# Kernel tuning notes

Measured on AMD Instinct MI355X. Metric: run time of the kernel, lower is better.

Reference implementation:

```python
import jax, jax.numpy as jnp
import numpy as np

N_NODES = 20000
N_EDGES = 240000
N_GRAPHS = 200
D_IN = 118
H = 256          # simplified hidden width standing in for the mul=50 irreps hidden
NB = 10          # number_of_basis
RH = 100         # fc_neurons hidden
L = 3            # layers
SH = 9           # lmax=2 -> 1+3+5 spherical-harmonic channels
MAX_RADIUS = 5.0
NUM_NEIGHBORS = 12.0


def setup_inputs() -> dict:
    key = jax.random.key(0)
    ks = jax.random.split(key, 16)
    inp = {
        "x": jax.random.normal(ks[0], (N_NODES, D_IN), jnp.float32),
        "pos": jax.random.normal(ks[1], (N_NODES, 3), jnp.float32),
        "edge_shift": jax.random.normal(ks[2], (N_EDGES, 3), jnp.float32),
        "lattice": jax.random.normal(ks[3], (N_GRAPHS, 3, 3), jnp.float32),
        "W_embed": jax.random.normal(ks[4], (D_IN, H), jnp.float32) / np.sqrt(D_IN),
        "r1": jax.random.normal(ks[5], (L, NB, RH), jnp.float32) / np.sqrt(NB),
        "b1": jax.random.normal(ks[6], (L, RH), jnp.float32) * 0.1,
        "r2": jax.random.normal(ks[7], (L, RH, H), jnp.float32) / np.sqrt(RH),
        "Wtp": jax.random.normal(ks[8], (L, SH, H, H), jnp.float32) / np.sqrt(SH * H),
        "Wself": jax.random.normal(ks[9], (L, H, H), jnp.float32) / np.sqrt(H),
        "Wskip": jax.random.normal(ks[10], (L, H, H), jnp.float32) / np.sqrt(H),
        "Wout": jax.random.normal(ks[11], (H, 1), jnp.float32) / np.sqrt(H),
        "edge_index": jax.random.randint(ks[12], (2, N_EDGES), 0, N_NODES, jnp.int64)
                        if jax.config.jax_enable_x64 else
                      jax.random.randint(ks[12], (2, N_EDGES), 0, N_NODES).astype(jnp.int32),
        "batch": jnp.sort(jax.random.randint(ks[13], (N_NODES,), 0, N_GRAPHS)).astype(jnp.int32),
    }
    return inp


def _sph_harm_lmax2(u):
    """Component-normalized real spherical harmonics up to l=2 on unit vectors u [E,3]."""
    x, y, z = u[:, 0], u[:, 1], u[:, 2]
    c1 = np.sqrt(3.0)
    c2 = np.sqrt(15.0)
    return jnp.stack([
        jnp.ones_like(x),                       # l=0
        c1 * x, c1 * y, c1 * z,                 # l=1
        c2 * x * y, c2 * y * z,                 # l=2
        (np.sqrt(5.0) / 2.0) * (3.0 * z * z - 1.0),
        c2 * x * z, (c2 / 2.0) * (x * x - y * y),
    ], axis=1)                                  # [E, 9]


def _soft_one_hot_cosine(lens):
    """e3nn soft_one_hot_linspace(basis='cosine', cutoff=True) * sqrt(NB)."""
    vals = jnp.linspace(0.0, MAX_RADIUS, NB + 2)
    step = vals[1] - vals[0]
    vals = vals[1:-1]
    diff = (lens[:, None] - vals[None, :]) / step          # [E, NB]
    emb = jnp.cos(0.5 * jnp.pi * diff) * (diff > -1.0) * (diff < 1.0)
    return emb * np.sqrt(float(NB))


def _forward(x, pos, edge_shift, lattice, W_embed, r1, b1, r2, Wtp, Wself, Wskip, Wout,
             edge_src, edge_dst, batch):
    edge_batch = batch[edge_src]                            # [E]
    # periodic edge vectors: pos[dst] - pos[src] + shift @ lattice[graph]
    edge_vec = pos[edge_dst] - pos[edge_src] + jnp.einsum(
        'ni,nij->nj', edge_shift, lattice[edge_batch])      # [E, 3]
    lens = jnp.linalg.norm(edge_vec, axis=1)                # [E]
    u = edge_vec / (lens[:, None] + 1e-12)
    sh = _sph_harm_lmax2(u)                                 # [E, 9]
    emb = _soft_one_hot_cosine(lens)                        # [E, NB]

    h = x @ W_embed                                         # [N, H]
    inv_sqrt_deg = 1.0 / np.sqrt(NUM_NEIGHBORS)
    for l in range(L):
        radial = jax.nn.silu(emb @ r1[l] + b1[l]) @ r2[l]   # [E, H]
        hs = h[edge_src] * radial                           # gather + radial gate
        # weighted tensor-product-like message: sum_a (hs * sh_a) @ Wtp[l, a]
        msg = (hs * sh[:, 0:1]) @ Wtp[l, 0]
        for a in range(1, SH):
            msg = msg + (hs * sh[:, a:a + 1]) @ Wtp[l, a]   # [E, H]
        agg = jax.ops.segment_sum(msg, edge_dst, num_segments=N_NODES) * inv_sqrt_deg
        h = jax.nn.gelu(agg @ Wself[l] + h @ Wskip[l])      # [N, H]

    node_out = h @ Wout                                     # [N, 1]
    # scatter_mean over graphs
    sums = jax.ops.segment_sum(node_out, batch, num_segments=N_GRAPHS)
    cnts = jax.ops.segment_sum(jnp.ones((N_NODES, 1), node_out.dtype), batch,
                               num_segments=N_GRAPHS)
    return sums / jnp.maximum(cnts, 1.0)                    # [G, 1]


def reference(x, pos, edge_shift, lattice, W_embed, r1, b1, r2, Wtp, Wself, Wskip, Wout,
              edge_index, batch):
    return _forward(x, pos, edge_shift, lattice, W_embed, r1, b1, r2, Wtp, Wself, Wskip,
                    Wout, edge_index[0], edge_index[1], batch)
```

## Files before the change

kernel.cpp:

```cpp
#include <hip/hip_runtime.h>
#include <hip/hip_bf16.h>
#include <cstddef>
#include <cstdint>

#define NNODE  20000
#define MPAD   20096
#define NEDGE  240000
#define NGRAPH 200
#define DIN    118
#define HD     256
#define NBASIS 10
#define RHID   100
#define NLAYER 3
#define NSH    9
#define SHSTR  16
#define KTP    (NSH * HD)
#define KTOT   (KTP + HD)
#define KR2    128
#define KEMB   128
#define NRT    (MPAD / 64)

typedef _Float16 f16;
typedef _Float16 f16x2 __attribute__((ext_vector_type(2)));
typedef _Float16 f16x4 __attribute__((ext_vector_type(4)));
typedef _Float16 f16x8 __attribute__((ext_vector_type(8)));
typedef float    f32x4 __attribute__((ext_vector_type(4)));

__device__ __forceinline__ float gelu_tanh(float v) {
  float v3 = v * v * v;
  return 0.5f * v * (1.f + tanhf(0.7978845608028654f * (v + 0.044715f * v3)));
}

__device__ __forceinline__ void gload16(const void* g, void* l) {
  __builtin_amdgcn_global_load_lds(
      (const __attribute__((address_space(1))) unsigned int*)g,
      (__attribute__((address_space(3))) unsigned int*)l, 16, 0, 0);
}

__device__ __forceinline__ int perm64(int rho) {
  return (rho & ~63) | ((rho & 15) * 4 + ((rho >> 4) & 3));
}
__device__ __forceinline__ int inv_perm64(int n) {
  return (n & ~63) | (((n & 3) << 4) | ((n >> 2) & 15));
}

__global__ void deg_hist_kernel(const int* __restrict__ ei, int* __restrict__ deg)
{
  int e = blockIdx.x * 256 + threadIdx.x;
  if (e >= NEDGE) return;
  atomicAdd(&deg[ei[NEDGE + e]], 1);
}

__global__ void scan_kernel(const int* __restrict__ deg, int* __restrict__ rowptr)
{
  __shared__ int part[256];
  int t = threadIdx.x;
  const int chunk = (NNODE + 255) / 256;
  int start = t * chunk;
  int end = min(start + chunk, NNODE);
  int s = 0;
  for (int i = start; i < end; ++i) s += deg[i];
  part[t] = s;
  __syncthreads();
  for (int off = 1; off < 256; off <<= 1) {
    int v = (t >= off) ? part[t - off] : 0;
    __syncthreads();
    part[t] += v;
    __syncthreads();
  }
  int run = (t == 0) ? 0 : part[t - 1];
  for (int i = start; i < end; ++i) { rowptr[i] = run; run += deg[i]; }
  if (t == 255) rowptr[NNODE] = run;
}

__global__ void edge_geom_kernel(const float* __restrict__ pos,
                                 const float* __restrict__ shift,
                                 const float* __restrict__ lat,
                                 const int* __restrict__ ei,
                                 const int* __restrict__ batch,
                                 const int* __restrict__ rowptr,
                                 int* __restrict__ cursor,
                                 f16* __restrict__ sh_s,
                                 float* __restrict__ lens_s)
{
  int e = blockIdx.x * 256 + threadIdx.x;
  if (e >= NEDGE) return;
  int src = ei[e];
  int dst = ei[NEDGE + e];
  int b = batch[src];
  const float* L = lat + (size_t)b * 9;
  float s0 = shift[e * 3 + 0], s1 = shift[e * 3 + 1], s2 = shift[e * 3 + 2];
  float ev[3];
#pragma unroll
  for (int j = 0; j < 3; ++j)
    ev[j] = pos[dst * 3 + j] - pos[src * 3 + j] + s0 * L[j] + s1 * L[3 + j] + s2 * L[6 + j];
  float len = sqrtf(ev[0] * ev[0] + ev[1] * ev[1] + ev[2] * ev[2]);
  float inv = 1.f / (len + 1e-12f);
  float x = ev[0] * inv, y = ev[1] * inv, z = ev[2] * inv;
  const float c1 = 1.7320508075688772f;
  const float c2 = 3.872983346207417f;
  int p = atomicAdd(&cursor[dst], 1);
  int si = rowptr[dst] + p;
  f16* she = sh_s + (size_t)si * SHSTR;
  she[0] = (f16)1.f;
  she[1] = (f16)(c1 * x);
  she[2] = (f16)(c1 * y);
  she[3] = (f16)(c1 * z);
  she[4] = (f16)(c2 * x * y);
  she[5] = (f16)(c2 * y * z);
  she[6] = (f16)(1.1180339887498949f * (3.f * z * z - 1.f));
  she[7] = (f16)(c2 * x * z);
  she[8] = (f16)(1.9364916731037085f * (x * x - y * y));
  she[9] = (f16)0.f;
  *(int*)(she + 10) = src;
  she[12] = (f16)0.f; she[13] = (f16)0.f; she[14] = (f16)0.f; she[15] = (f16)0.f;
  lens_s[si] = len;
}

__global__ void prep_kernel(const float* __restrict__ Wtp_l,
                            const float* __restrict__ Wself_l,
                            const float* __restrict__ Wskip_l,
                            const float* __restrict__ r2l,
                            const float* __restrict__ r1l,
                            const float* __restrict__ b1l,
                            f16* __restrict__ Wtp16,
                            f16* __restrict__ WselfT16,
                            f16* __restrict__ Bcat,
                            f16* __restrict__ r2h,
                            f16* __restrict__ r1h)
{
  int b = blockIdx.x, t = threadIdx.x;
  if (b < KTP) {
    int i = b * 256 + t;
    Wtp16[i] = (f16)Wtp_l[i];
  } else if (b < KTP + 256) {
    int n = b - KTP;
    WselfT16[(size_t)n * HD + t] = (f16)(Wself_l[(size_t)t * HD + n] * 0.28867513459481287f);
  } else if (b < KTP + 512) {
    int rho = b - KTP - 256;
    int pcol = perm64(rho);
    Bcat[(size_t)rho * KTOT + KTP + t] = (f16)Wskip_l[(size_t)t * HD + pcol];
  } else if (b < KTP + 768) {
    int rho = b - KTP - 512;
    if (t < KR2) {
      int p = perm64(rho);
      r2h[(size_t)rho * KR2 + t] = (t < RHID) ? (f16)r2l[(size_t)t * HD + p] : (f16)0.f;
    }
  } else {
#pragma unroll
    for (int u = 0; u < 16; ++u) {
      int idx = u * 256 + t;
      int n = idx >> 5, j = idx & 31;
      float v = 0.f;
      if (n < RHID) {
        if (j < NBASIS) v = r1l[(size_t)j * RHID + n];
        else if (j == NBASIS) v = b1l[n];
      }
      r1h[idx] = (f16)v;
    }
  }
}

__global__ void convert_x_kernel(const float* __restrict__ x, f16* __restrict__ xh)
{
  int i = blockIdx.x * 2 + (threadIdx.x >> 7);
  int k = threadIdx.x & 127;
  xh[(size_t)i * KEMB + k] = (i < NNODE && k < DIN) ? (f16)x[(size_t)i * DIN + k] : (f16)0.f;
}

__global__ void convert_wemb_kernel(const float* __restrict__ Wemb, f16* __restrict__ WembT16)
{
  int n = blockIdx.x, k = threadIdx.x;
  WembT16[(size_t)n * KEMB + k] = (k < DIN) ? (f16)Wemb[(size_t)k * HD + n] : (f16)0.f;
}

__global__ __launch_bounds__(256) void gemm_nt_kernel(
    const f16* __restrict__ A, const f16* __restrict__ B,
    f16* __restrict__ C, int K, int ldc, int permRows)
{
  __shared__ __align__(16) f16 As[4][64][8];
  __shared__ __align__(16) f16 Bs[4][128][8];
  int t = threadIdx.x;
  int lane = t & 63, w = t >> 6;
  int row0 = blockIdx.x * 64;
  int n0 = blockIdx.y * 128;
  f32x4 acc[2][4];
#pragma unroll
  for (int i = 0; i < 2; ++i)
#pragma unroll
    for (int j = 0; j < 4; ++j) acc[i][j] = (f32x4){0.f, 0.f, 0.f, 0.f};
  int mq = (w & 1) * 32, nq = (w >> 1) * 64;
  for (int k0 = 0; k0 < K; k0 += 32) {
    {
      int row = t & 63, cc = t >> 6;
      *(uint4*)&As[cc][row][0] = *(const uint4*)(A + (size_t)(row0 + row) * K + k0 + cc * 8);
    }
#pragma unroll
    for (int u = 0; u < 2; ++u) {
      int idx = t + u * 256;
      int ch = idx >> 7, nn = idx & 127;
      *(uint4*)&Bs[ch][nn][0] = *(const uint4*)(B + (size_t)(n0 + nn) * K + k0 + ch * 8);
    }
    __syncthreads();
    int q = lane >> 4, r = lane & 15;
    f16x8 af[2], bfr[4];
#pragma unroll
    for (int i = 0; i < 2; ++i) af[i] = *(const f16x8*)&As[q][mq + i * 16 + r][0];
#pragma unroll
    for (int j = 0; j < 4; ++j) bfr[j] = *(const f16x8*)&Bs[q][nq + j * 16 + r][0];
#pragma unroll
    for (int i = 0; i < 2; ++i)
#pragma unroll
      for (int j = 0; j < 4; ++j)
        acc[i][j] = __builtin_amdgcn_mfma_f32_16x16x32_f16(af[i], bfr[j], acc[i][j], 0, 0, 0);
    __syncthreads();
  }
  int q4 = ((lane >> 4)) * 4, cl = lane & 15;
#pragma unroll
  for (int i = 0; i < 2; ++i)
#pragma unroll
    for (int rr = 0; rr < 4; ++rr) {
      int row = row0 + mq + i * 16 + q4 + rr;
      int orow = permRows ? inv_perm64(row) : row;
#pragma unroll
      for (int j = 0; j < 4; ++j)
        C[(size_t)orow * ldc + n0 + nq + j * 16 + cl] = (f16)acc[i][j][rr];
    }
}

#define RHSTR 136
__global__ __launch_bounds__(256) void radial_kernel(
    const float* __restrict__ lens_s,
    const f16* __restrict__ r1h,
    const f16* __restrict__ r2h,
    f16* __restrict__ rad)
{
  __shared__ __align__(16) f16 emb_s[64][40];
  __shared__ __align__(16) f16 rhA[64 * RHSTR];
  int t = threadIdx.x;
  int lane = t & 63, w = t >> 6;
  int r = lane & 15, q = lane >> 4;
  int e0 = blockIdx.x * 64;

  {
    float len = lens_s[e0 + lane];
    const float step = 5.f / 11.f;
    const float sq = 3.1622776601683795f;
    f16x8 v;
#pragma unroll
    for (int kk = 0; kk < 8; ++kk) {
      int j = w * 8 + kk;
      float val = 0.f;
      if (j < NBASIS) {
        float d = (len - (float)(j + 1) * step) / step;
        val = (d > -1.f && d < 1.f) ? (__cosf(1.5707963267948966f * d) * sq) : 0.f;
      } else if (j == NBASIS) {
        val = 1.f;
      }
      v[kk] = (f16)val;
    }
    *(f16x8*)&emb_s[lane][w * 8] = v;
  }

  int n0w = w * 64;
  f16x8 bfr[4][4];
#pragma unroll
  for (int j = 0; j < 4; ++j)
#pragma unroll
    for (int ks = 0; ks < 4; ++ks)
      bfr[j][ks] = *(const f16x8*)(r2h + (size_t)(n0w + j * 16 + r) * KR2 + ks * 32 + q * 8);

  f16x8 b1f[2];
#pragma unroll
  for (int j = 0; j < 2; ++j)
    b1f[j] = *(const f16x8*)(r1h + (size_t)((2 * w + j) * 16 + r) * 32 + q * 8);

  __syncthreads();

  f32x4 acc1[4][2];
#pragma unroll
  for (int i = 0; i < 4; ++i)
#pragma unroll
    for (int j = 0; j < 2; ++j) acc1[i][j] = (f32x4){0.f, 0.f, 0.f, 0.f};
  {
    f16x8 a1f[4];
#pragma unroll
    for (int i = 0; i < 4; ++i)
      a1f[i] = *(const f16x8*)&emb_s[i * 16 + r][q * 8];
#pragma unroll
    for (int i = 0; i < 4; ++i)
#pragma unroll
      for (int j = 0; j < 2; ++j)
        acc1[i][j] = __builtin_amdgcn_mfma_f32_16x16x32_f16(a1f[i], b1f[j], acc1[i][j], 0, 0, 0);
  }

#pragma unroll
  for (int i = 0; i < 4; ++i)
#pragma unroll
    for (int j = 0; j < 2; ++j)
#pragma unroll
      for (int rr = 0; rr < 4; ++rr) {
        float s = acc1[i][j][rr];
        s = __fdividef(s, 1.f + __expf(-s));
        rhA[(i * 16 + q * 4 + rr) * RHSTR + (2 * w + j) * 16 + r] = (f16)s;
      }
  __syncthreads();

  f32x4 acc[4][4];
#pragma unroll
  for (int i = 0; i < 4; ++i)
#pragma unroll
    for (int j = 0; j < 4; ++j) acc[i][j] = (f32x4){0.f, 0.f, 0.f, 0.f};
#pragma unroll
  for (int ks = 0; ks < 4; ++ks) {
    f16x8 af[4];
#pragma unroll
    for (int i = 0; i < 4; ++i)
      af[i] = *(const f16x8*)&rhA[(i * 16 + r) * RHSTR + ks * 32 + q * 8];
#pragma unroll
    for (int i = 0; i < 4; ++i)
#pragma unroll
      for (int j = 0; j < 4; ++j)
        acc[i][j] = __builtin_amdgcn_mfma_f32_16x16x32_f16(af[i], bfr[j][ks], acc[i][j], 0, 0, 0);
  }

#pragma unroll
  for (int i = 0; i < 4; ++i)
#pragma unroll
    for (int rr = 0; rr < 4; ++rr) {
      int m = i * 16 + q * 4 + rr;
      f16x4 o;
#pragma unroll
      for (int j = 0; j < 4; ++j) o[j] = (f16)acc[i][j][rr];
      *(f16x4*)(rad + (size_t)(e0 + m) * HD + n0w + r * 4) = o;
    }
}

__global__ __launch_bounds__(256) void gather2_kernel(
    const int* __restrict__ rowptr, const f16* __restrict__ rad,
    const f16* __restrict__ h, const f16* __restrict__ sh_s,
    f16* __restrict__ T)
{
  int t = threadIdx.x;
  int half = t >> 7, lc = t & 127;
  int base = blockIdx.x * 4;
  for (int s = 0; s < 2; ++s) {
    int n = base + s * 2 + half;
    int beg = rowptr[n], end = rowptr[n + 1];
    float a0[NSH], a1[NSH];
#pragma unroll
    for (int a = 0; a < NSH; ++a) { a0[a] = 0.f; a1[a] = 0.f; }
    int j = beg;
    for (; j + 2 <= end; j += 2) {
      const f16* she0 = sh_s + (size_t)j * SHSTR;
      const f16* she1 = she0 + SHSTR;
      f16x8 s80 = *(const f16x8*)she0;
      f16x8 s81 = *(const f16x8*)she1;
      float s8v0 = (float)she0[8];
      float s8v1 = (float)she1[8];
      int src0 = *(const int*)(she0 + 10);
      int src1 = *(const int*)(she1 + 10);
      f16x2 rv0 = *(const f16x2*)(rad + (size_t)j * HD + 2 * lc);
      f16x2 rv1 = *(const f16x2*)(rad + (size_t)(j + 1) * HD + 2 * lc);
      f16x2 hv0 = *(const f16x2*)(h + (size_t)src0 * HD + 2 * lc);
      f16x2 hv1 = *(const f16x2*)(h + (size_t)src1 * HD + 2 * lc);
      float p00 = (float)rv0[0] * (float)hv0[0];
      float p01 = (float)rv0[1] * (float)hv0[1];
      float p10 = (float)rv1[0] * (float)hv1[0];
      float p11 = (float)rv1[1] * (float)hv1[1];
#pragma unroll
      for (int a = 0; a < 8; ++a) {
        float sv0 = (float)s80[a], sv1 = (float)s81[a];
        a0[a] += sv0 * p00 + sv1 * p10;
        a1[a] += sv0 * p01 + sv1 * p11;
      }
      a0[8] += s8v0 * p00 + s8v1 * p10;
      a1[8] += s8v0 * p01 + s8v1 * p11;
    }
    if (j < end) {
      const f16* she = sh_s + (size_t)j * SHSTR;
      f16x8 s8 = *(const f16x8*)she;
      float s8v = (float)she[8];
      int src = *(const int*)(she + 10);
      f16x2 rv = *(const f16x2*)(rad + (size_t)j * HD + 2 * lc);
      f16x2 hv = *(const f16x2*)(h + (size_t)src * HD + 2 * lc);
      float p0 = (float)rv[0] * (float)hv[0];
      float p1 = (float)rv[1] * (float)hv[1];
#pragma unroll
      for (int a = 0; a < 8; ++a) {
        float sv = (float)s8[a];
        a0[a] += sv * p0; a1[a] += sv * p1;
      }
      a0[8] += s8v * p0; a1[8] += s8v * p1;
    }
    f16* Tn = T + (size_t)n * KTP + 2 * lc;
#pragma unroll
    for (int a = 0; a < NSH; ++a) {
      f16x2 o; o[0] = (f16)a0[a]; o[1] = (f16)a1[a];
      *(f16x2*)(Tn + a * HD) = o;
    }
  }
}

#define GBM 64
#define GBN 128
#define NKSTEP (KTOT / 32)
#define NBUF 4
__global__ __launch_bounds__(256) void gemm_fused_kernel(
    const f16* __restrict__ A1,
    const f16* __restrict__ A2,
    const f16* __restrict__ B,
    f16* __restrict__ C)
{
  __shared__ __align__(16) f16 As[NBUF][GBM][4][8];
  __shared__ __align__(16) f16 Bs[NBUF][GBN][4][8];
  int t = threadIdx.x;
  int lane = t & 63, w = t >> 6;
  int row0 = blockIdx.x * GBM;
  int n0 = blockIdx.y * GBN;
  int mq = (w & 1) * 32, nq = (w >> 1) * 64;
  int q = lane >> 4, r = lane & 15;

  int arow = t >> 2;
  int ach = (t & 3) ^ ((t >> 3) & 3);

  f32x4 acc[2][4];
#pragma unroll
  for (int i = 0; i < 2; ++i)
#pragma unroll
    for (int j = 0; j < 4; ++j) acc[i][j] = (f32x4){0.f, 0.f, 0.f, 0.f};

  auto stage = [&](int buf, int k0) {
    const f16* ga = (k0 < KTP)
        ? (A1 + (size_t)(row0 + arow) * KTP + k0 + ach * 8)
        : (A2 + (size_t)(row0 + arow) * HD + (k0 - KTP) + ach * 8);
    gload16(ga, (f16*)As + (size_t)buf * (GBM * 32) + w * 512);
#pragma unroll
    for (int u = 0; u < 2; ++u) {
      int idx = t + u * 256;
      int brow = idx >> 2;
      int bch = (idx & 3) ^ ((idx >> 3) & 3);
      const f16* gb = B + (size_t)(n0 + brow) * KTOT + k0 + bch * 8;
      gload16(gb, (f16*)Bs + (size_t)buf * (GBN * 32) + (u * 256 + w * 64) * 8);
    }
  };

  stage(0, 0);
  stage(1, 32);
  stage(2, 64);

  int swz = (q ^ ((r >> 1) & 3)) * 8;
  int cur = 0;
  for (int s = 0; s < NKSTEP; ++s) {
    if (s <= NKSTEP - 3)      asm volatile("s_waitcnt vmcnt(6)" ::: "memory");
    else if (s == NKSTEP - 2) asm volatile("s_waitcnt vmcnt(3)" ::: "memory");
    else                      asm volatile("s_waitcnt vmcnt(0)" ::: "memory");
    __builtin_amdgcn_s_barrier();
    if (s + 3 < NKSTEP) stage((cur + 3) & 3, (s + 3) * 32);

    const f16* As_c = (const f16*)As + (size_t)cur * (GBM * 32);
    const f16* Bs_c = (const f16*)Bs + (size_t)cur * (GBN * 32);
    f16x8 af[2], bfr[4];
#pragma unroll
    for (int i = 0; i < 2; ++i)
      af[i] = *(const f16x8*)(As_c + (mq + i * 16 + r) * 32 + swz);
#pragma unroll
    for (int j = 0; j < 4; ++j)
      bfr[j] = *(const f16x8*)(Bs_c + (nq + j * 16 + r) * 32 + swz);
#pragma unroll
    for (int i = 0; i < 2; ++i)
#pragma unroll
      for (int j = 0; j < 4; ++j)
        acc[i][j] = __builtin_amdgcn_mfma_f32_16x16x32_f16(af[i], bfr[j], acc[i][j], 0, 0, 0);
    cur = (cur + 1) & 3;
  }

  int q4 = (lane >> 4) * 4, cl = lane & 15;
#pragma unroll
  for (int i = 0; i < 2; ++i)
#pragma unroll
    for (int rr = 0; rr < 4; ++rr) {
      int row = row0 + mq + i * 16 + q4 + rr;
      f16x4 o;
#pragma unroll
      for (int j = 0; j < 4; ++j) o[j] = (f16)gelu_tanh(acc[i][j][rr]);
      *(f16x4*)(C + (size_t)row * HD + n0 + nq + cl * 4) = o;
    }
}

__global__ __launch_bounds__(256) void node_out_fused_kernel(
    const f16* __restrict__ h,
    const float* __restrict__ Wout,
    const int* __restrict__ batch,
    float* __restrict__ out)
{
  __shared__ float red[256];
  int g = blockIdx.x;
  int t = threadIdx.x;
  int lo = 0, hi = NNODE;
  while (lo < hi) { int mid = (lo + hi) >> 1; if (batch[mid] < g) lo = mid + 1; else hi = mid; }
  int start = lo;
  hi = NNODE;
  while (lo < hi) { int mid = (lo + hi) >> 1; if (batch[mid] < g + 1) lo = mid + 1; else hi = mid; }
  int end = lo;
  int half = t >> 7, lc = t & 127;
  float a0 = 0.f, a1 = 0.f;
  for (int n = start + half; n < end; n += 2) {
    f16x2 v = *(const f16x2*)(h + (size_t)n * HD + 2 * lc);
    a0 += (float)v[0];
    a1 += (float)v[1];
  }
  red[t] = a0 * Wout[2 * lc] + a1 * Wout[2 * lc + 1];
  for (int off = 128; off > 0; off >>= 1) {
    __syncthreads();
    if (t < off) red[t] += red[t + off];
  }
  if (t == 0) out[g] = red[0] / fmaxf((float)(end - start), 1.f);
}

extern "C" void kernel_launch(void* const* d_in, const int* in_sizes, int n_in,
                              void* d_out, int out_size, void* d_ws, size_t ws_size,
                              hipStream_t stream)
{
  (void)in_sizes; (void)n_in; (void)out_size;
  const float* x     = (const float*)d_in[0];
  const float* pos   = (const float*)d_in[1];
  const float* shift = (const float*)d_in[2];
  const float* lat   = (const float*)d_in[3];
  const float* Wemb  = (const float*)d_in[4];
  const float* r1    = (const float*)d_in[5];
  const float* b1    = (const float*)d_in[6];
  const float* r2    = (const float*)d_in[7];
  const float* Wtp   = (const float*)d_in[8];
  const float* Wself = (const float*)d_in[9];
  const float* Wskip = (const float*)d_in[10];
  const float* Wout  = (const float*)d_in[11];
  const int*   eidx  = (const int*)d_in[12];
  const int*   batch = (const int*)d_in[13];
  float* out = (float*)d_out;

  char* ws = (char*)d_ws;
  size_t off = 0;
  auto alloc = [&](size_t bytes) -> char* {
    char* p = ws + off;
    off += (bytes + 255) & ~(size_t)255;
    return p;
  };
  f16*   sh_s    = (f16*)alloc((size_t)NEDGE * SHSTR * 2);
  float* lens_s  = (float*)alloc((size_t)NEDGE * 4);
  f16*   hA      = (f16*)alloc((size_t)MPAD * HD * 2);
  f16*   hB      = (f16*)alloc((size_t)MPAD * HD * 2);
  f16*   T       = (f16*)alloc((size_t)MPAD * KTP * 2);
  f16*   rad     = (f16*)alloc((size_t)NEDGE * HD * 2);
  f16*   Bcat    = (f16*)alloc((size_t)HD * KTOT * 2);
  f16*   r2h     = (f16*)alloc((size_t)HD * KR2 * 2);
  f16*   r1hb    = (f16*)alloc((size_t)128 * 32 * 2);
  f16*   Wtp16   = (f16*)alloc((size_t)KTP * HD * 2);
  f16*   WselfT16= (f16*)alloc((size_t)HD * HD * 2);
  int*   rowptr  = (int*)alloc((size_t)(NNODE + 1) * 4);
  int*   deg     = (int*)alloc((size_t)NNODE * 4);
  int*   cursor  = (int*)alloc((size_t)NNODE * 4);
  if (off > ws_size) return;

  f16*   xh      = rad;
  f16*   WembT16 = rad + (size_t)MPAD * KEMB;

  hipMemsetAsync(deg, 0, (size_t)NNODE * 4, stream);
  hipMemsetAsync(cursor, 0, (size_t)NNODE * 4, stream);

  const int EB = (NEDGE + 255) / 256;
  deg_hist_kernel<<<EB, 256, 0, stream>>>(eidx, deg);
  scan_kernel<<<1, 256, 0, stream>>>(deg, rowptr);
  edge_geom_kernel<<<EB, 256, 0, stream>>>(pos, shift, lat, eidx, batch,
                                           rowptr, cursor, sh_s, lens_s);

  convert_x_kernel<<<MPAD / 2, 256, 0, stream>>>(x, xh);
  convert_wemb_kernel<<<HD, KEMB, 0, stream>>>(Wemb, WembT16);
  {
    dim3 eg(MPAD / 64, HD / 128);
    gemm_nt_kernel<<<eg, 256, 0, stream>>>(xh, WembT16, hA, KEMB, HD, 0);
  }

  f16* hcur = hA;
  f16* hnxt = hB;
  dim3 fgrid(NRT, 2);
  dim3 wgrid(HD / 64, KTP / 128);
  for (int l = 0; l < NLAYER; ++l) {
    const float* r1l = r1 + (size_t)l * NBASIS * RHID;
    const float* b1l = b1 + (size_t)l * RHID;
    const float* r2l = r2 + (size_t)l * RHID * HD;
    const float* Wtp_l = Wtp + (size_t)l * NSH * HD * HD;
    const float* Wself_l = Wself + (size_t)l * HD * HD;
    const float* Wskip_l = Wskip + (size_t)l * HD * HD;

    prep_kernel<<<KTP + 768 + 1, 256, 0, stream>>>(Wtp_l, Wself_l, Wskip_l, r2l,
                                                   r1l, b1l,
                                                   Wtp16, WselfT16, Bcat, r2h, r1hb);
    gemm_nt_kernel<<<wgrid, 256, 0, stream>>>(WselfT16, Wtp16, Bcat, HD, KTOT, 1);

    radial_kernel<<<NEDGE / 64, 256, 0, stream>>>(lens_s, r1hb, r2h, rad);
    gather2_kernel<<<NNODE / 4, 256, 0, stream>>>(rowptr, rad, hcur, sh_s, T);
    gemm_fused_kernel<<<fgrid, 256, 0, stream>>>(T, hcur, Bcat, hnxt);
    f16* tmp = hcur; hcur = hnxt; hnxt = tmp;
  }

  node_out_fused_kernel<<<NGRAPH, 256, 0, stream>>>(hcur, Wout, batch, out);
}
```

Before: 718.4 us.

## Fuse neighbor feature gather into radial kernel and simplify GEMM to double buffer

The radial MLP kernel now loads each edge's source-node features and multiplies them into the radial weights, writing the gated per-edge product directly. The aggregation kernel then reads only this product, removing its separate indexed gather of node features. Separately, the fused GEMM's four-stage async pipeline with explicit vmcnt waits is replaced by a simple two-buffer scheme with block barriers. This reduces LDS use but weakens latency hiding and may lack a wait for async LDS loads.

```diff
diff --git a/kernel.cpp b/kernel.cpp
--- a/kernel.cpp
+++ b/kernel.cpp
@@ -231,16 +231,21 @@
 #define RHSTR 136
 __global__ __launch_bounds__(256) void radial_kernel(
     const float* __restrict__ lens_s,
+    const f16* __restrict__ sh_s,
+    const f16* __restrict__ h,
     const f16* __restrict__ r1h,
     const f16* __restrict__ r2h,
-    f16* __restrict__ rad)
+    f16* __restrict__ hs)
 {
   __shared__ __align__(16) f16 emb_s[64][40];
   __shared__ __align__(16) f16 rhA[64 * RHSTR];
+  __shared__ int srcs[64];
   int t = threadIdx.x;
   int lane = t & 63, w = t >> 6;
   int r = lane & 15, q = lane >> 4;
   int e0 = blockIdx.x * 64;
+
+  if (t < 64) srcs[t] = *(const int*)(sh_s + (size_t)(e0 + t) * SHSTR + 10);
 
   {
     float len = lens_s[e0 + lane];
@@ -306,6 +311,15 @@
       }
   __syncthreads();
 
+  f16x4 hv[4][4];
+#pragma unroll
+  for (int i = 0; i < 4; ++i)
+#pragma unroll
+    for (int rr = 0; rr < 4; ++rr) {
+      int m = i * 16 + q * 4 + rr;
+      hv[i][rr] = *(const f16x4*)(h + (size_t)srcs[m] * HD + n0w + r * 4);
+    }
+
   f32x4 acc[4][4];
 #pragma unroll
   for (int i = 0; i < 4; ++i)
@@ -331,14 +345,15 @@
       int m = i * 16 + q * 4 + rr;
       f16x4 o;
 #pragma unroll
-      for (int j = 0; j < 4; ++j) o[j] = (f16)acc[i][j][rr];
-      *(f16x4*)(rad + (size_t)(e0 + m) * HD + n0w + r * 4) = o;
+      for (int j = 0; j < 4; ++j)
+        o[j] = (f16)(acc[i][j][rr] * (float)hv[i][rr][j]);
+      *(f16x4*)(hs + (size_t)(e0 + m) * HD + n0w + r * 4) = o;
     }
 }
 
 __global__ __launch_bounds__(256) void gather2_kernel(
-    const int* __restrict__ rowptr, const f16* __restrict__ rad,
-    const f16* __restrict__ h, const f16* __restrict__ sh_s,
+    const int* __restrict__ rowptr, const f16* __restrict__ hs,
+    const f16* __restrict__ sh_s,
     f16* __restrict__ T)
 {
   int t = threadIdx.x;
@@ -358,16 +373,12 @@
       f16x8 s81 = *(const f16x8*)she1;
       float s8v0 = (float)she0[8];
       float s8v1 = (float)she1[8];
-      int src0 = *(const int*)(she0 + 10);
-      int src1 = *(const int*)(she1 + 10);
-      f16x2 rv0 = *(const f16x2*)(rad + (size_t)j * HD + 2 * lc);
-      f16x2 rv1 = *(const f16x2*)(rad + (size_t)(j + 1) * HD + 2 * lc);
-      f16x2 hv0 = *(const f16x2*)(h + (size_t)src0 * HD + 2 * lc);
-      f16x2 hv1 = *(const f16x2*)(h + (size_t)src1 * HD + 2 * lc);
-      float p00 = (float)rv0[0] * (float)hv0[0];
-      float p01 = (float)rv0[1] * (float)hv0[1];
-      float p10 = (float)rv1[0] * (float)hv1[0];
-      float p11 = (float)rv1[1] * (float)hv1[1];
+      f16x2 rv0 = *(const f16x2*)(hs + (size_t)j * HD + 2 * lc);
+      f16x2 rv1 = *(const f16x2*)(hs + (size_t)(j + 1) * HD + 2 * lc);
+      float p00 = (float)rv0[0];
+      float p01 = (float)rv0[1];
+      float p10 = (float)rv1[0];
+      float p11 = (float)rv1[1];
 #pragma unroll
       for (int a = 0; a < 8; ++a) {
         float sv0 = (float)s80[a], sv1 = (float)s81[a];
@@ -381,11 +392,9 @@
       const f16* she = sh_s + (size_t)j * SHSTR;
       f16x8 s8 = *(const f16x8*)she;
       float s8v = (float)she[8];
-      int src = *(const int*)(she + 10);
-      f16x2 rv = *(const f16x2*)(rad + (size_t)j * HD + 2 * lc);
-      f16x2 hv = *(const f16x2*)(h + (size_t)src * HD + 2 * lc);
-      float p0 = (float)rv[0] * (float)hv[0];
-      float p1 = (float)rv[1] * (float)hv[1];
+      f16x2 rv = *(const f16x2*)(hs + (size_t)j * HD + 2 * lc);
+      float p0 = (float)rv[0];
+      float p1 = (float)rv[1];
 #pragma unroll
       for (int a = 0; a < 8; ++a) {
         float sv = (float)s8[a];
@@ -405,15 +414,14 @@
 #define GBM 64
 #define GBN 128
 #define NKSTEP (KTOT / 32)
-#define NBUF 4
 __global__ __launch_bounds__(256) void gemm_fused_kernel(
     const f16* __restrict__ A1,
     const f16* __restrict__ A2,
     const f16* __restrict__ B,
     f16* __restrict__ C)
 {
-  __shared__ __align__(16) f16 As[NBUF][GBM][4][8];
-  __shared__ __align__(16) f16 Bs[NBUF][GBN][4][8];
+  __shared__ __align__(16) f16 As[2][GBM][4][8];
+  __shared__ __align__(16) f16 Bs[2][GBN][4][8];
   int t = threadIdx.x;
   int lane = t & 63, w = t >> 6;
   int row0 = blockIdx.x * GBM;
@@ -446,18 +454,12 @@
   };
 
   stage(0, 0);
-  stage(1, 32);
-  stage(2, 64);
+  __syncthreads();
 
   int swz = (q ^ ((r >> 1) & 3)) * 8;
   int cur = 0;
   for (int s = 0; s < NKSTEP; ++s) {
-    if (s <= NKSTEP - 3)      asm volatile("s_waitcnt vmcnt(6)" ::: "memory");
-    else if (s == NKSTEP - 2) asm volatile("s_waitcnt vmcnt(3)" ::: "memory");
-    else                      asm volatile("s_waitcnt vmcnt(0)" ::: "memory");
-    __builtin_amdgcn_s_barrier();
-    if (s + 3 < NKSTEP) stage((cur + 3) & 3, (s + 3) * 32);
-
+    if (s + 1 < NKSTEP) stage(cur ^ 1, (s + 1) * 32);
     const f16* As_c = (const f16*)As + (size_t)cur * (GBM * 32);
     const f16* Bs_c = (const f16*)Bs + (size_t)cur * (GBN * 32);
     f16x8 af[2], bfr[4];
@@ -472,7 +474,8 @@
 #pragma unroll
       for (int j = 0; j < 4; ++j)
         acc[i][j] = __builtin_amdgcn_mfma_f32_16x16x32_f16(af[i], bfr[j], acc[i][j], 0, 0, 0);
-    cur = (cur + 1) & 3;
+    __syncthreads();
+    cur ^= 1;
   }
 
   int q4 = (lane >> 4) * 4, cl = lane & 15;
@@ -598,8 +601,8 @@
                                                    Wtp16, WselfT16, Bcat, r2h, r1hb);
     gemm_nt_kernel<<<wgrid, 256, 0, stream>>>(WselfT16, Wtp16, Bcat, HD, KTOT, 1);
 
-    radial_kernel<<<NEDGE / 64, 256, 0, stream>>>(lens_s, r1hb, r2h, rad);
-    gather2_kernel<<<NNODE / 4, 256, 0, stream>>>(rowptr, rad, hcur, sh_s, T);
+    radial_kernel<<<NEDGE / 64, 256, 0, stream>>>(lens_s, sh_s, hcur, r1hb, r2h, rad);
+    gather2_kernel<<<NNODE / 4, 256, 0, stream>>>(rowptr, rad, sh_s, T);
     gemm_fused_kernel<<<fgrid, 256, 0, stream>>>(T, hcur, Bcat, hnxt);
     f16* tmp = hcur; hcur = hnxt; hnxt = tmp;
   }
```

New measurement: 704.7 us. About the same (-1.9%).
